# Kernel tuning notes

Hardware: AMD Instinct MI355X
Metric: run time of the kernel (lower is better)

Reference implementation:

```python
import jax, jax.numpy as jnp
import numpy as np

B, S, D = 4, 2048, 2048
H = 16
DH = D // H  # 128


def setup_inputs() -> dict:
    key = jax.random.key(0)
    ks = jax.random.split(key, 12)
    s = 1.0 / np.sqrt(D)
    inp = {
        "Q": jax.random.normal(ks[0], (B, S, D), jnp.float32),
        "K": jax.random.normal(ks[1], (B, S, D), jnp.float32),
        "V": jax.random.normal(ks[2], (B, S, D), jnp.float32),
        "mask": jnp.tril(jnp.ones((S, S), jnp.int32))[None, None],  # causal [1,1,S,S]
        "wq": jax.random.uniform(ks[3], (D, D), jnp.float32, -s, s),
        "bq": jax.random.uniform(ks[4], (D,), jnp.float32, -s, s),
        "wk": jax.random.uniform(ks[5], (D, D), jnp.float32, -s, s),
        "bk": jax.random.uniform(ks[6], (D,), jnp.float32, -s, s),
        "wv": jax.random.uniform(ks[7], (D, D), jnp.float32, -s, s),
        "bv": jax.random.uniform(ks[8], (D,), jnp.float32, -s, s),
        "wo": jax.random.uniform(ks[9], (D, D), jnp.float32, -s, s),
        "bo": jax.random.uniform(ks[10], (D,), jnp.float32, -s, s),
    }
    return inp


def _split_heads(x):
    # [B,S,D] -> [B,H,S,DH]
    b, s, _ = x.shape
    return x.reshape(b, s, H, DH).transpose(0, 2, 1, 3)


def reference(Q, K, V, mask, wq, bq, wk, bk, wv, bv, wo, bo):
    q = _split_heads(Q @ wq + bq)
    k = _split_heads(K @ wk + bk)
    v = _split_heads(V @ wv + bv)
    scores = jnp.einsum("bhqd,bhkd->bhqk", q, k) / jnp.sqrt(jnp.float32(DH))
    scores = jnp.where(mask == 0, jnp.float32(-1e9), scores)
    probs = jax.nn.softmax(scores, axis=-1)
    attn = jnp.einsum("bhqk,bhkd->bhqd", probs, v)  # [B,H,S,DH]
    attn = attn.transpose(0, 2, 1, 3).reshape(Q.shape[0], Q.shape[1], D)
    return attn @ wo + bo
```

## Files before the change

kernel.cpp:

```cpp
#include <hip/hip_runtime.h>
#include <hip/hip_bf16.h>

typedef __attribute__((ext_vector_type(8))) short short8;
typedef __attribute__((ext_vector_type(4))) float f32x4;

#define DEVINL __device__ __forceinline__

constexpr int Bc = 4, Sc = 2048, Dc = 2048, Hc = 16, DHc = 128;
constexpr float SCALE = 0.08838834764831845f;

DEVINL short f2bf(float f) {
  unsigned u = __builtin_bit_cast(unsigned, f);
  u = (u + 0x7fffu + ((u >> 16) & 1u)) >> 16;
  return (short)u;
}
DEVINL unsigned pack2(float a, float b) {
  return (unsigned)(unsigned short)f2bf(a) | ((unsigned)(unsigned short)f2bf(b) << 16);
}

DEVINL void gload16(const void* g, void* l) {
  __builtin_amdgcn_global_load_lds(
      (const __attribute__((address_space(1))) void*)g,
      (__attribute__((address_space(3))) void*)l, 16, 0, 0);
}

__global__ __launch_bounds__(256) void transpose_w_kernel(
    const float* __restrict__ w0, const float* __restrict__ w1,
    const float* __restrict__ w2, const float* __restrict__ w3,
    short* __restrict__ wt) {
  __shared__ float tile[32][33];
  const float* w = (blockIdx.z == 0) ? w0 : (blockIdx.z == 1) ? w1
                   : (blockIdx.z == 2) ? w2 : w3;
  short* out = wt + (size_t)blockIdx.z * Dc * Dc;
  int k0 = blockIdx.x * 32, n0 = blockIdx.y * 32;
  int t = threadIdx.x;
#pragma unroll
  for (int p = 0; p < 4; ++p) {
    int idx = p * 256 + t;
    int kr = idx >> 5, nc = idx & 31;
    tile[kr][nc] = w[(size_t)(k0 + kr) * Dc + n0 + nc];
  }
  __syncthreads();
#pragma unroll
  for (int p = 0; p < 4; ++p) {
    int idx = p * 256 + t;
    int nr = idx >> 5, kc = idx & 31;
    out[(size_t)(n0 + nr) * Dc + k0 + kc] = f2bf(tile[kc][nr]);
  }
}

__global__ __launch_bounds__(256) void convert_kernel(
    const float* __restrict__ in, short* __restrict__ out, int n8) {
  int stride = gridDim.x * 256;
  for (int idx = blockIdx.x * 256 + threadIdx.x; idx < n8; idx += stride) {
    const f32x4* p = (const f32x4*)(in + (size_t)idx * 8);
    f32x4 a = p[0], b = p[1];
    short8 r;
    r[0] = f2bf(a[0]); r[1] = f2bf(a[1]); r[2] = f2bf(a[2]); r[3] = f2bf(a[3]);
    r[4] = f2bf(b[0]); r[5] = f2bf(b[1]); r[6] = f2bf(b[2]); r[7] = f2bf(b[3]);
    *(short8*)(out + (size_t)idx * 8) = r;
  }
}

template <int OUT_MODE>
__global__ __launch_bounds__(512, 2) void gemm_ring_kernel(
    const short* __restrict__ A, const short* __restrict__ Wt,
    const float* __restrict__ bias, void* __restrict__ Cptr) {
  __shared__ __align__(16) short As[4][256 * 32];
  __shared__ __align__(16) short Bs[4][256 * 32];
  const int tid = threadIdx.x, lane = tid & 63, wid = tid >> 6;
  const int wm = wid >> 2, wn = wid & 3;
  const int lr = lane & 15, g = lane >> 4;
  const int physg = (g ^ ((lr >> 1) & 3)) * 8;

  const int bid = blockIdx.x;
  const int swz = (bid & 7) * 32 + (bid >> 3);
  const int m0 = (swz >> 3) * 256, n0 = (swz & 7) * 256;

  const int srow = lane >> 2;
  const int scol = ((lane & 3) ^ ((lane >> 3) & 3)) * 8;
  const size_t abase = (size_t)(m0 + wid * 32 + srow) * Dc + scol;
  const size_t bbase = (size_t)(n0 + wid * 32 + srow) * Dc + scol;
  const int ldof = wid * 32 * 64;

  auto stageA = [&](int kt) {
    const short* src = &A[abase + kt * 32];
    char* dst = (char*)&As[kt & 3][0] + ldof;
    gload16(src, dst);
    gload16(src + (size_t)16 * Dc, dst + 16 * 64);
  };
  auto stageB = [&](int kt) {
    const short* src = &Wt[bbase + kt * 32];
    char* dst = (char*)&Bs[kt & 3][0] + ldof;
    gload16(src, dst);
    gload16(src + (size_t)16 * Dc, dst + 16 * 64);
  };

  f32x4 acc[8][4] = {};

  stageA(0); stageB(0);
  stageA(1); stageB(1);
  stageA(2); stageB(2);
  asm volatile("s_waitcnt vmcnt(8)" ::: "memory");
  __builtin_amdgcn_s_barrier();

  for (int kt = 0; kt < 64; ++kt) {
    const short* Ab = &As[kt & 3][0];
    const short* Bb = &Bs[kt & 3][0];
    short8 afr[4], bfr[4];

#pragma unroll
    for (int i = 0; i < 4; ++i)
      afr[i] = *(const short8*)&Ab[(wm * 128 + i * 16 + lr) * 32 + physg];
#pragma unroll
    for (int j = 0; j < 4; ++j)
      bfr[j] = *(const short8*)&Bb[(wn * 64 + j * 16 + lr) * 32 + physg];
    if (kt < 61) stageA(kt + 3);
    __builtin_amdgcn_s_barrier();
    asm volatile("s_waitcnt lgkmcnt(0)" ::: "memory");
    __builtin_amdgcn_sched_barrier(0);
    __builtin_amdgcn_s_setprio(1);
#pragma unroll
    for (int i = 0; i < 4; ++i)
#pragma unroll
      for (int j = 0; j < 4; ++j)
        acc[i][j] = __builtin_amdgcn_mfma_f32_16x16x32_bf16(afr[i], bfr[j], acc[i][j], 0, 0, 0);
    __builtin_amdgcn_s_setprio(0);
    __builtin_amdgcn_s_barrier();

#pragma unroll
    for (int i = 0; i < 4; ++i)
      afr[i] = *(const short8*)&Ab[(wm * 128 + 64 + i * 16 + lr) * 32 + physg];
    if (kt < 61) stageB(kt + 3);
    __builtin_amdgcn_s_barrier();
    asm volatile("s_waitcnt lgkmcnt(0)" ::: "memory");
    __builtin_amdgcn_sched_barrier(0);
    __builtin_amdgcn_s_setprio(1);
#pragma unroll
    for (int i = 0; i < 4; ++i)
#pragma unroll
      for (int j = 0; j < 4; ++j)
        acc[4 + i][j] = __builtin_amdgcn_mfma_f32_16x16x32_bf16(afr[i], bfr[j], acc[4 + i][j], 0, 0, 0);
    __builtin_amdgcn_s_setprio(0);
    if (kt <= 60) {
      asm volatile("s_waitcnt vmcnt(8)" ::: "memory");
    } else if (kt == 61) {
      asm volatile("s_waitcnt vmcnt(4)" ::: "memory");
    } else if (kt == 62) {
      asm volatile("s_waitcnt vmcnt(0)" ::: "memory");
    }
    __builtin_amdgcn_s_barrier();
  }

  const int rowl = g * 4;
#pragma unroll
  for (int bj = 0; bj < 4; ++bj) {
    const int gcol = n0 + wn * 64 + bj * 16 + lr;
    const float bv = bias[gcol];
#pragma unroll
    for (int ai = 0; ai < 8; ++ai) {
#pragma unroll
      for (int r = 0; r < 4; ++r) {
        int grow = m0 + wm * 128 + ai * 16 + rowl + r;
        float v = acc[ai][bj][r] + bv;
        if (OUT_MODE == 1) {
          ((float*)Cptr)[(size_t)grow * Dc + gcol] = v;
        } else if (OUT_MODE == 0) {
          ((short*)Cptr)[(size_t)grow * Dc + gcol] = f2bf(v);
        } else {
          int b4 = grow >> 11, ss = grow & (Sc - 1);
          int hh = gcol >> 7, dh = gcol & (DHc - 1);
          ((short*)Cptr)[((((size_t)(b4 * Hc + hh) * DHc) + dh) << 11) + ss] = f2bf(v);
        }
      }
    }
  }
}

__global__ __launch_bounds__(512, 2) void attn_kernel(
    const short* __restrict__ qp, const short* __restrict__ kp,
    const short* __restrict__ vt, short* __restrict__ attn) {
  __shared__ __align__(16) short Ks[64 * 128];
  __shared__ __align__(16) short Vs[128 * 64];
  __shared__ __align__(16) short Ps[8][32][72];
  const int tid = threadIdx.x, lane = tid & 63, wid = tid >> 6;
  const int lr = lane & 15, g = lane >> 4, lk = g * 8, rowl = g * 4;
  const int d = blockIdx.x;
  const int xcd = d & 7, s = d >> 3;
  const int grp = s >> 3;
  const int qi = (grp < 4) ? grp : 11 - grp;
  const int bh = xcd * 8 + (s & 7);
  const int b = bh >> 4, h = bh & 15;
  const int qb = qi * 256;
  const size_t headq = ((size_t)b * Sc) * Dc + (size_t)h * DHc;
  const size_t vbase = (((size_t)b * Hc + h) * DHc) << 11;
  const int qw = qb + wid * 32;
  const int x7 = lr & 7;

  short8 qf[2][4];
#pragma unroll
  for (int qs = 0; qs < 2; ++qs)
#pragma unroll
    for (int c = 0; c < 4; ++c)
      qf[qs][c] = *(const short8*)&qp[headq + (size_t)(qw + qs * 16 + lr) * Dc + c * 32 + lk];

  const int krow = wid * 4 + g;
  const int kcol = lr * 8;
  const int vrow = wid * 8 + (lane >> 3);
  const int vcol = (lane & 7) * 8;
  int kdst[2], vdst[2];
#pragma unroll
  for (int p = 0; p < 2; ++p) {
    int kr = p * 32 + krow;
    kdst[p] = kr * 128 + ((lr ^ (kr & 7)) * 8);
    int vr = p * 64 + vrow;
    vdst[p] = vr * 64 + (((lane & 7) ^ (vr & 7)) * 8);
  }

  short8 kreg[2], vreg[2];
  auto issue = [&](int kvb) {
#pragma unroll
    for (int p = 0; p < 2; ++p)
      kreg[p] = *(const short8*)&kp[headq + (size_t)(kvb + p * 32 + krow) * Dc + kcol];
#pragma unroll
    for (int p = 0; p < 2; ++p)
      vreg[p] = *(const short8*)&vt[vbase + (size_t)(p * 64 + vrow) * Sc + kvb + vcol];
  };
  auto commit = [&]() {
#pragma unroll
    for (int p = 0; p < 2; ++p) *(short8*)&Ks[kdst[p]] = kreg[p];
#pragma unroll
    for (int p = 0; p < 2; ++p) *(short8*)&Vs[vdst[p]] = vreg[p];
  };

  issue(0);
  commit();
  __syncthreads();

  f32x4 o[2][8] = {};
  float mrun[2] = {-1e30f, -1e30f}, lrun[2] = {0.f, 0.f};
  const int ntiles = qb / 64 + 4;

  for (int t = 0; t < ntiles; ++t) {
    const bool active = (64 * t <= qw + 31);
    f32x4 sc[2][4];

    if (active) {
      __builtin_amdgcn_s_setprio(1);
#pragma unroll
      for (int nb = 0; nb < 4; ++nb) {
        f32x4 s0 = {}, s1 = {};
#pragma unroll
        for (int c = 0; c < 4; ++c) {
          short8 kf = *(const short8*)&Ks[(nb * 16 + lr) * 128 + (((c * 4 + g) ^ x7) << 3)];
          s0 = __builtin_amdgcn_mfma_f32_16x16x32_bf16(kf, qf[0][c], s0, 0, 0, 0);
          s1 = __builtin_amdgcn_mfma_f32_16x16x32_bf16(kf, qf[1][c], s1, 0, 0, 0);
        }
        sc[0][nb] = s0;
        sc[1][nb] = s1;
      }
      __builtin_amdgcn_s_setprio(0);
    }

    if (t + 1 < ntiles) issue((t + 1) * 64);

    if (active) {
      const bool domask = (64 * t + 63 > qw);
#pragma unroll
      for (int qs = 0; qs < 2; ++qs) {
        const int qg = qw + qs * 16 + lr;
        float mnb[4];
#pragma unroll
        for (int nb = 0; nb < 4; ++nb) {
#pragma unroll
          for (int r = 0; r < 4; ++r) {
            float v = sc[qs][nb][r] * SCALE;
            if (domask) {
              int kv = t * 64 + nb * 16 + rowl + r;
              v = (kv > qg) ? -1e30f : v;
            }
            sc[qs][nb][r] = v;
          }
          mnb[nb] = fmaxf(fmaxf(sc[qs][nb][0], sc[qs][nb][1]),
                          fmaxf(sc[qs][nb][2], sc[qs][nb][3]));
        }
        float mt = fmaxf(fmaxf(mnb[0], mnb[1]), fmaxf(mnb[2], mnb[3]));
        mt = fmaxf(mt, __shfl_xor(mt, 16));
        mt = fmaxf(mt, __shfl_xor(mt, 32));

        float mnew = fmaxf(mrun[qs], mt);
        float alpha = __expf(mrun[qs] - mnew);
        mrun[qs] = mnew;

        float lsnb[4];
#pragma unroll
        for (int nb = 0; nb < 4; ++nb) {
          float p0 = __expf(sc[qs][nb][0] - mnew);
          float p1 = __expf(sc[qs][nb][1] - mnew);
          float p2 = __expf(sc[qs][nb][2] - mnew);
          float p3 = __expf(sc[qs][nb][3] - mnew);
          lsnb[nb] = (p0 + p1) + (p2 + p3);
          uint2 w;
          w.x = pack2(p0, p1);
          w.y = pack2(p2, p3);
          *(uint2*)&Ps[wid][qs * 16 + lr][nb * 16 + rowl] = w;
        }
        float ls = (lsnb[0] + lsnb[1]) + (lsnb[2] + lsnb[3]);
        ls += __shfl_xor(ls, 16);
        ls += __shfl_xor(ls, 32);
        lrun[qs] = lrun[qs] * alpha + ls;

        float al[4];
#pragma unroll
        for (int r = 0; r < 4; ++r) al[r] = __shfl(alpha, (lane & 48) | (rowl + r));
#pragma unroll
        for (int f = 0; f < 8; ++f)
#pragma unroll
          for (int r = 0; r < 4; ++r) o[qs][f][r] *= al[r];
      }

      asm volatile("s_waitcnt lgkmcnt(0)" ::: "memory");
      __builtin_amdgcn_sched_barrier(0);

      __builtin_amdgcn_s_setprio(1);
#pragma unroll
      for (int kc = 0; kc < 2; ++kc) {
        short8 pf0 = *(const short8*)&Ps[wid][lr][kc * 32 + lk];
        short8 pf1 = *(const short8*)&Ps[wid][16 + lr][kc * 32 + lk];
#pragma unroll
        for (int nb = 0; nb < 8; ++nb) {
          short8 vf = *(const short8*)&Vs[(nb * 16 + lr) * 64 + (((kc * 4 + g) ^ x7) << 3)];
          o[0][nb] = __builtin_amdgcn_mfma_f32_16x16x32_bf16(pf0, vf, o[0][nb], 0, 0, 0);
          o[1][nb] = __builtin_amdgcn_mfma_f32_16x16x32_bf16(pf1, vf, o[1][nb], 0, 0, 0);
        }
      }
      __builtin_amdgcn_s_setprio(0);
    }

    __syncthreads();
    if (t + 1 < ntiles) commit();
    __syncthreads();
  }

#pragma unroll
  for (int qs = 0; qs < 2; ++qs) {
    float ld[4];
#pragma unroll
    for (int r = 0; r < 4; ++r) ld[r] = __shfl(lrun[qs], (lane & 48) | (rowl + r));
#pragma unroll
    for (int f = 0; f < 8; ++f)
#pragma unroll
      for (int r = 0; r < 4; ++r) {
        float v = o[qs][f][r] / ld[r];
        attn[headq + (size_t)(qw + qs * 16 + rowl + r) * Dc + f * 16 + lr] = f2bf(v);
      }
  }
}

extern "C" void kernel_launch(void* const* d_in, const int* in_sizes, int n_in,
                              void* d_out, int out_size, void* d_ws, size_t ws_size,
                              hipStream_t stream) {
  const float* Q = (const float*)d_in[0];
  const float* K = (const float*)d_in[1];
  const float* V = (const float*)d_in[2];
  const float* wq = (const float*)d_in[4];
  const float* bq = (const float*)d_in[5];
  const float* wk = (const float*)d_in[6];
  const float* bk = (const float*)d_in[7];
  const float* wv = (const float*)d_in[8];
  const float* bv = (const float*)d_in[9];
  const float* wo = (const float*)d_in[10];
  const float* bo = (const float*)d_in[11];

  char* ws = (char*)d_ws;
  const size_t WSZ = (size_t)Dc * Dc;
  const size_t XSZ = (size_t)Bc * Sc * Dc;
  short* WT = (short*)ws;
  short* QP = (short*)(ws + 4 * WSZ * 2);
  short* KP = (short*)(ws + 4 * WSZ * 2 + XSZ * 2);
  short* VT = (short*)(ws + 4 * WSZ * 2 + 2 * XSZ * 2);
  short* AT = (short*)(ws + 4 * WSZ * 2 + 3 * XSZ * 2);

  transpose_w_kernel<<<dim3(Dc / 32, Dc / 32, 4), 256, 0, stream>>>(wq, wk, wv, wo, WT);

  const int n8 = (int)(XSZ / 8);
  const int ng = (Bc * Sc / 256) * (Dc / 256);

  convert_kernel<<<2048, 256, 0, stream>>>(Q, AT, n8);
  gemm_ring_kernel<0><<<ng, 512, 0, stream>>>(AT, WT, bq, QP);
  convert_kernel<<<2048, 256, 0, stream>>>(K, AT, n8);
  gemm_ring_kernel<0><<<ng, 512, 0, stream>>>(AT, WT + WSZ, bk, KP);
  convert_kernel<<<2048, 256, 0, stream>>>(V, AT, n8);
  gemm_ring_kernel<2><<<ng, 512, 0, stream>>>(AT, WT + 2 * WSZ, bv, VT);

  attn_kernel<<<512, 512, 0, stream>>>(QP, KP, VT, AT);

  gemm_ring_kernel<1><<<ng, 512, 0, stream>>>(AT, WT + 3 * WSZ, bo, (float*)d_out);
}
```

Before: 499.6 us.

## Restructure GEMM main loop to one barrier per k-step; use exp2 in softmax

The GEMM main loop now waits on global loads and synchronises once per k-tile, reads all A/B fragments up front, issues both stage loads, then runs all 32 MFMAs back to back. This replaces the earlier two-phase pattern with four barriers per step. Launch bounds drop from two blocks to one per CU, which raises the register budget but may cut occupancy. In attention, the softmax folds log2(e) into the scale and uses the hardware exp2 instruction instead of __expf, which removes a multiply per exponential.

```diff
diff --git a/kernel.cpp b/kernel.cpp
--- a/kernel.cpp
+++ b/kernel.cpp
@@ -7,7 +7,9 @@
 #define DEVINL __device__ __forceinline__
 
 constexpr int Bc = 4, Sc = 2048, Dc = 2048, Hc = 16, DHc = 128;
-constexpr float SCALE = 0.08838834764831845f;
+constexpr float SCALE2 = 0.08838834764831845f * 1.4426950408889634f;
+
+DEVINL float exp2s(float x) { return __builtin_amdgcn_exp2f(x); }
 
 DEVINL short f2bf(float f) {
   unsigned u = __builtin_bit_cast(unsigned, f);
@@ -63,7 +65,7 @@
 }
 
 template <int OUT_MODE>
-__global__ __launch_bounds__(512, 2) void gemm_ring_kernel(
+__global__ __launch_bounds__(512, 1) void gemm_ring_kernel(
     const short* __restrict__ A, const short* __restrict__ Wt,
     const float* __restrict__ bias, void* __restrict__ Cptr) {
   __shared__ __align__(16) short As[4][256 * 32];
@@ -101,55 +103,45 @@
   stageA(0); stageB(0);
   stageA(1); stageB(1);
   stageA(2); stageB(2);
-  asm volatile("s_waitcnt vmcnt(8)" ::: "memory");
-  __builtin_amdgcn_s_barrier();
 
   for (int kt = 0; kt < 64; ++kt) {
-    const short* Ab = &As[kt & 3][0];
-    const short* Bb = &Bs[kt & 3][0];
-    short8 afr[4], bfr[4];
-
-#pragma unroll
-    for (int i = 0; i < 4; ++i)
-      afr[i] = *(const short8*)&Ab[(wm * 128 + i * 16 + lr) * 32 + physg];
-#pragma unroll
-    for (int j = 0; j < 4; ++j)
-      bfr[j] = *(const short8*)&Bb[(wn * 64 + j * 16 + lr) * 32 + physg];
-    if (kt < 61) stageA(kt + 3);
-    __builtin_amdgcn_s_barrier();
-    asm volatile("s_waitcnt lgkmcnt(0)" ::: "memory");
-    __builtin_amdgcn_sched_barrier(0);
-    __builtin_amdgcn_s_setprio(1);
-#pragma unroll
-    for (int i = 0; i < 4; ++i)
-#pragma unroll
-      for (int j = 0; j < 4; ++j)
-        acc[i][j] = __builtin_amdgcn_mfma_f32_16x16x32_bf16(afr[i], bfr[j], acc[i][j], 0, 0, 0);
-    __builtin_amdgcn_s_setprio(0);
-    __builtin_amdgcn_s_barrier();
-
-#pragma unroll
-    for (int i = 0; i < 4; ++i)
-      afr[i] = *(const short8*)&Ab[(wm * 128 + 64 + i * 16 + lr) * 32 + physg];
-    if (kt < 61) stageB(kt + 3);
-    __builtin_amdgcn_s_barrier();
-    asm volatile("s_waitcnt lgkmcnt(0)" ::: "memory");
-    __builtin_amdgcn_sched_barrier(0);
-    __builtin_amdgcn_s_setprio(1);
-#pragma unroll
-    for (int i = 0; i < 4; ++i)
-#pragma unroll
-      for (int j = 0; j < 4; ++j)
-        acc[4 + i][j] = __builtin_amdgcn_mfma_f32_16x16x32_bf16(afr[i], bfr[j], acc[4 + i][j], 0, 0, 0);
-    __builtin_amdgcn_s_setprio(0);
-    if (kt <= 60) {
+    if (kt < 62) {
       asm volatile("s_waitcnt vmcnt(8)" ::: "memory");
-    } else if (kt == 61) {
+    } else if (kt == 62) {
       asm volatile("s_waitcnt vmcnt(4)" ::: "memory");
-    } else if (kt == 62) {
+    } else {
       asm volatile("s_waitcnt vmcnt(0)" ::: "memory");
     }
     __builtin_amdgcn_s_barrier();
+    asm volatile("" ::: "memory");
+
+    const short* Ab = &As[kt & 3][0];
+    const short* Bb = &Bs[kt & 3][0];
+    short8 afr[4], bfr[4], af2[4];
+#pragma unroll
+    for (int i = 0; i < 4; ++i)
+      afr[i] = *(const short8*)&Ab[(wm * 128 + i * 16 + lr) * 32 + physg];
+#pragma unroll
+    for (int j = 0; j < 4; ++j)
+      bfr[j] = *(const short8*)&Bb[(wn * 64 + j * 16 + lr) * 32 + physg];
+#pragma unroll
+    for (int i = 0; i < 4; ++i)
+      af2[i] = *(const short8*)&Ab[(wm * 128 + 64 + i * 16 + lr) * 32 + physg];
+
+    if (kt <= 60) { stageA(kt + 3); stageB(kt + 3); }
+
+    __builtin_amdgcn_s_setprio(1);
+#pragma unroll
+    for (int i = 0; i < 4; ++i)
+#pragma unroll
+      for (int j = 0; j < 4; ++j)
+        acc[i][j] = __builtin_amdgcn_mfma_f32_16x16x32_bf16(afr[i], bfr[j], acc[i][j], 0, 0, 0);
+#pragma unroll
+    for (int i = 0; i < 4; ++i)
+#pragma unroll
+      for (int j = 0; j < 4; ++j)
+        acc[4 + i][j] = __builtin_amdgcn_mfma_f32_16x16x32_bf16(af2[i], bfr[j], acc[4 + i][j], 0, 0, 0);
+    __builtin_amdgcn_s_setprio(0);
   }
 
   const int rowl = g * 4;
@@ -274,7 +266,7 @@
         for (int nb = 0; nb < 4; ++nb) {
 #pragma unroll
           for (int r = 0; r < 4; ++r) {
-            float v = sc[qs][nb][r] * SCALE;
+            float v = sc[qs][nb][r] * SCALE2;
             if (domask) {
               int kv = t * 64 + nb * 16 + rowl + r;
               v = (kv > qg) ? -1e30f : v;
@@ -289,16 +281,16 @@
         mt = fmaxf(mt, __shfl_xor(mt, 32));
 
         float mnew = fmaxf(mrun[qs], mt);
-        float alpha = __expf(mrun[qs] - mnew);
+        float alpha = exp2s(mrun[qs] - mnew);
         mrun[qs] = mnew;
 
         float lsnb[4];
 #pragma unroll
         for (int nb = 0; nb < 4; ++nb) {
-          float p0 = __expf(sc[qs][nb][0] - mnew);
-          float p1 = __expf(sc[qs][nb][1] - mnew);
-          float p2 = __expf(sc[qs][nb][2] - mnew);
-          float p3 = __expf(sc[qs][nb][3] - mnew);
+          float p0 = exp2s(sc[qs][nb][0] - mnew);
+          float p1 = exp2s(sc[qs][nb][1] - mnew);
+          float p2 = exp2s(sc[qs][nb][2] - mnew);
+          float p3 = exp2s(sc[qs][nb][3] - mnew);
           lsnb[nb] = (p0 + p1) + (p2 + p3);
           uint2 w;
           w.x = pack2(p0, p1);
```

Measured after the change: 475.3 us. 1.05x faster.
